# Optimization experiments

Hardware: AMD Instinct MI355X
Metric: run time of the kernel (lower is better)

Reference implementation:

```python
import jax, jax.numpy as jnp
import numpy as np

DIM = 1024
N_HEAD = 16
HEAD_DIM = DIM // N_HEAD
HIDDEN = 4 * DIM
EPS = 1e-6
NEG = -1e9


def setup_inputs() -> dict:
    key = jax.random.key(0)
    ks = jax.random.split(key, 9)
    B, T = 2, 2048
    x = jax.random.normal(ks[0], (B, T, DIM), dtype=jnp.float32)
    # additive causal mask [T, T]
    mask = jnp.where(jnp.tril(jnp.ones((T, T), dtype=bool)), 0.0, NEG).astype(jnp.float32)
    s = 0.02
    wq = jax.random.normal(ks[1], (DIM, DIM), dtype=jnp.float32) * s
    wk = jax.random.normal(ks[2], (DIM, DIM), dtype=jnp.float32) * s
    wv = jax.random.normal(ks[3], (DIM, DIM), dtype=jnp.float32) * s
    wo = jax.random.normal(ks[4], (DIM, DIM), dtype=jnp.float32) * s
    w1 = jax.random.normal(ks[5], (DIM, HIDDEN), dtype=jnp.float32) * s
    w2 = jax.random.normal(ks[6], (HIDDEN, DIM), dtype=jnp.float32) * s
    g_attn = jnp.ones((DIM,), dtype=jnp.float32)
    g_ffn = jnp.ones((DIM,), dtype=jnp.float32)
    return {"x": x, "mask": mask, "wq": wq, "wk": wk, "wv": wv, "wo": wo,
            "w1": w1, "w2": w2, "g_attn": g_attn, "g_ffn": g_ffn}


def _rmsnorm(x, g):
    norm = jax.lax.rsqrt(jnp.mean(jnp.square(x), axis=-1, keepdims=True) + EPS)
    return (x * norm) * g


def _attention(x, mask, wq, wk, wv, wo):
    B, T, C = x.shape
    # project and split heads: [B, H, T, D]
    q = (x @ wq).reshape(B, T, N_HEAD, HEAD_DIM).transpose(0, 2, 1, 3)
    k = (x @ wk).reshape(B, T, N_HEAD, HEAD_DIM).transpose(0, 2, 1, 3)
    v = (x @ wv).reshape(B, T, N_HEAD, HEAD_DIM).transpose(0, 2, 1, 3)
    attn = jnp.einsum('bhtd,bhsd->bhts', q, k) / np.sqrt(HEAD_DIM).astype(np.float32)
    attn = attn + mask  # broadcast [T,T] over [B,H,T,T]
    p = jax.nn.softmax(attn, axis=-1)
    out = jnp.einsum('bhts,bhsd->bhtd', p, v)
    out = out.transpose(0, 2, 1, 3).reshape(B, T, C)
    return out @ wo


def reference(x, mask, wq, wk, wv, wo, w1, w2, g_attn, g_ffn):
    x = x + _attention(_rmsnorm(x, g_attn), mask, wq, wk, wv, wo)
    h = _rmsnorm(x, g_ffn)
    return x + (jax.nn.silu(h @ w1) @ w2)
```

## Files before the change

### kernel.cpp

```cpp
#include <hip/hip_runtime.h>
#include <hip/hip_bf16.h>
#include <cstdint>
#include <cstddef>

#define DIM    1024
#define NHEAD  16
#define HDIM   64
#define HIDDEN 4096
#define TSEQ   2048
#define TOKENS 4096

typedef __attribute__((ext_vector_type(4))) float  f32x4;
typedef __attribute__((ext_vector_type(8))) short  short8;
typedef __attribute__((ext_vector_type(8))) __bf16 bf16x8;

__device__ __forceinline__ short f2bf(float f) {
    union { float f; uint32_t u; } v; v.f = f;
    uint32_t u = v.u;
    uint32_t r = (u + 0x7fffu + ((u >> 16) & 1u)) >> 16;
    return (short)r;
}

__device__ __forceinline__ float bf2f(short s) {
    uint32_t u = ((uint32_t)(uint16_t)s) << 16;
    return __builtin_bit_cast(float, u);
}

__device__ __forceinline__ f32x4 mfma_bf16(short8 a, short8 b, f32x4 c) {
    return __builtin_amdgcn_mfma_f32_16x16x32_bf16(
        __builtin_bit_cast(bf16x8, a), __builtin_bit_cast(bf16x8, b), c, 0, 0, 0);
}

__device__ __forceinline__ void barrier_lds() {
    asm volatile("s_waitcnt lgkmcnt(0)\n\ts_barrier" ::: "memory");
}

__global__ __launch_bounds__(256) void transpose_w(
    const float* __restrict__ W, short* __restrict__ Wt, int K, int N)
{
    __shared__ float tile[64][65];
    const int tid = threadIdx.x;
    const int n0 = blockIdx.x * 64, k0 = blockIdx.y * 64;
    for (int i = tid; i < 4096; i += 256) {
        int r = i >> 6, c = i & 63;
        tile[r][c] = W[(size_t)(k0 + r) * N + n0 + c];
    }
    __syncthreads();
    for (int i = tid; i < 4096; i += 256) {
        int r = i >> 6, c = i & 63;
        Wt[(size_t)(n0 + r) * K + k0 + c] = f2bf(tile[c][r]);
    }
}

__global__ __launch_bounds__(256) void transpose_v(
    const short* __restrict__ qkv, short* __restrict__ Vt)
{
    __shared__ short tile[64][72];
    const int tid = threadIdx.x;
    const int s0 = blockIdx.x * 64, bh = blockIdx.y;
    const int b = bh >> 4, h = bh & 15;
    const short* src = qkv + ((size_t)(b * TSEQ + s0)) * 3072 + 2048 + h * 64;
    for (int i = tid; i < 512; i += 256) {
        int r = i >> 3, cg = i & 7;
        *(short8*)&tile[r][cg * 8] = *(const short8*)(src + (size_t)r * 3072 + cg * 8);
    }
    __syncthreads();
    short* dst = Vt + ((size_t)bh * 64) * TSEQ + s0;
    for (int i = tid; i < 512; i += 256) {
        int d = i >> 3, sg = i & 7;
        short8 o;
#pragma unroll
        for (int j = 0; j < 8; ++j) o[j] = tile[sg * 8 + j][d];
        *(short8*)(dst + (size_t)d * TSEQ + sg * 8) = o;
    }
}

__global__ __launch_bounds__(256) void rmsnorm_k(
    const float* __restrict__ x, const float* __restrict__ g, short* __restrict__ out)
{
    const int t = blockIdx.x, tid = threadIdx.x;
    const int wave = tid >> 6, lane = tid & 63;
    const float4 v = ((const float4*)(x + (size_t)t * DIM))[tid];
    float ss = v.x * v.x + v.y * v.y + v.z * v.z + v.w * v.w;
#pragma unroll
    for (int d = 1; d < 64; d <<= 1) ss += __shfl_xor(ss, d, 64);
    __shared__ float red[4];
    if (lane == 0) red[wave] = ss;
    __syncthreads();
    float tot = red[0] + red[1] + red[2] + red[3];
    float rn = rsqrtf(tot * (1.0f / (float)DIM) + 1e-6f);
    const float4 gv = ((const float4*)g)[tid];
    short4 ov = make_short4(f2bf(v.x * rn * gv.x), f2bf(v.y * rn * gv.y),
                            f2bf(v.z * rn * gv.z), f2bf(v.w * rn * gv.w));
    ((short4*)(out + (size_t)t * DIM))[tid] = ov;
}

template <int EPI>
__global__ __launch_bounds__(256) void gemm_bt(
    const short* __restrict__ A, const short* __restrict__ Bt,
    void* __restrict__ Cout, const float* __restrict__ res,
    int M, int N, int K)
{
    __shared__ short As[128 * 64];
    __shared__ short Bs[128 * 64];
    const int tid  = threadIdx.x;
    const int wave = tid >> 6, lane = tid & 63;
    const int lm = lane & 15, quad = lane >> 4;
    const int wm = wave & 1, wn = wave >> 1;
    const int m0 = blockIdx.x * 128, n0 = blockIdx.y * 128;
    const int Ksl = K / gridDim.z;
    const int kbeg = blockIdx.z * Ksl;
    const int nIter = Ksl >> 6;

    const f32x4 zero = {0.f, 0.f, 0.f, 0.f};
    f32x4 acc[4][4];
#pragma unroll
    for (int i = 0; i < 4; ++i)
#pragma unroll
        for (int j = 0; j < 4; ++j) acc[i][j] = zero;

    const int srow = tid >> 3;
    const int scol = (tid & 7) * 8;
    const int pcol = ((tid & 7) ^ (srow & 7)) * 8;
    const short* Ap = A + (size_t)(m0 + srow) * K + kbeg + scol;
    const short* Bp = Bt + (size_t)(n0 + srow) * K + kbeg + scol;

    short8 ar[4], br[4];

    auto loadtile = [&]() {
#pragma unroll
        for (int j = 0; j < 4; ++j) {
            ar[j] = *(const short8*)(Ap + (size_t)(j * 32) * K);
            br[j] = *(const short8*)(Bp + (size_t)(j * 32) * K);
        }
        Ap += 64; Bp += 64;
    };

    auto storetile = [&]() {
#pragma unroll
        for (int j = 0; j < 4; ++j) {
            *(short8*)&As[(srow + j * 32) * 64 + pcol] = ar[j];
            *(short8*)&Bs[(srow + j * 32) * 64 + pcol] = br[j];
        }
    };

    const int e = lm & 7;
    auto compute = [&]() {
#pragma unroll
        for (int kk = 0; kk < 2; ++kk) {
            short8 af[4], bf[4];
#pragma unroll
            for (int mt = 0; mt < 4; ++mt)
                af[mt] = *(const short8*)&As[(wm * 64 + mt * 16 + lm) * 64 +
                                             ((((kk << 2) | quad) ^ e) << 3)];
#pragma unroll
            for (int nt = 0; nt < 4; ++nt)
                bf[nt] = *(const short8*)&Bs[(wn * 64 + nt * 16 + lm) * 64 +
                                             ((((kk << 2) | quad) ^ e) << 3)];
#pragma unroll
            for (int mt = 0; mt < 4; ++mt)
#pragma unroll
                for (int nt = 0; nt < 4; ++nt)
                    acc[mt][nt] = mfma_bf16(af[mt], bf[nt], acc[mt][nt]);
        }
    };

    loadtile();

    for (int it = 0; it < nIter; ++it) {
        barrier_lds();
        storetile();
        barrier_lds();
        if (it + 1 < nIter) loadtile();
        compute();
    }

#pragma unroll
    for (int mt = 0; mt < 4; ++mt) {
#pragma unroll
        for (int r = 0; r < 4; ++r) {
            const int row = m0 + wm * 64 + mt * 16 + quad * 4 + r;
#pragma unroll
            for (int nt = 0; nt < 4; ++nt) {
                const int col = n0 + wn * 64 + nt * 16 + lm;
                const size_t idx = (size_t)row * N + col;
                const float v = acc[mt][nt][r];
                if constexpr (EPI == 0) {
                    ((short*)Cout)[idx] = f2bf(v);
                } else if constexpr (EPI == 1) {
                    ((float*)Cout)[idx] = res[idx] + v;
                } else if constexpr (EPI == 2) {
                    ((short*)Cout)[idx] = f2bf(v / (1.0f + __expf(-v)));
                } else {
                    ((short*)Cout)[(size_t)blockIdx.z * M * N + idx] = f2bf(v);
                }
            }
        }
    }
}

__global__ __launch_bounds__(256) void combine_k4(
    const short* __restrict__ p, const float* __restrict__ res,
    float* __restrict__ out, int n)
{
    const int i = blockIdx.x * 256 + threadIdx.x;
    if (i * 4 < n) {
        float4 v = ((const float4*)res)[i];
#pragma unroll
        for (int s = 0; s < 4; ++s) {
            short4 ps = ((const short4*)(p + (size_t)s * n))[i];
            v.x += bf2f(ps.x); v.y += bf2f(ps.y);
            v.z += bf2f(ps.z); v.w += bf2f(ps.w);
        }
        ((float4*)out)[i] = v;
    }
}

__global__ __launch_bounds__(256) void combine_rms4(
    const short* __restrict__ p, const float* __restrict__ res,
    const float* __restrict__ g, float* __restrict__ x2out,
    short* __restrict__ nout)
{
    const int t = blockIdx.x, tid = threadIdx.x;
    const int wave = tid >> 6, lane = tid & 63;
    const size_t i4 = (size_t)t * 256 + tid;
    float4 v = ((const float4*)res)[i4];
#pragma unroll
    for (int s = 0; s < 4; ++s) {
        short4 ps = ((const short4*)(p + (size_t)s * TOKENS * DIM))[i4];
        v.x += bf2f(ps.x); v.y += bf2f(ps.y);
        v.z += bf2f(ps.z); v.w += bf2f(ps.w);
    }
    ((float4*)x2out)[i4] = v;
    float ss = v.x * v.x + v.y * v.y + v.z * v.z + v.w * v.w;
#pragma unroll
    for (int d = 1; d < 64; d <<= 1) ss += __shfl_xor(ss, d, 64);
    __shared__ float red[4];
    if (lane == 0) red[wave] = ss;
    __syncthreads();
    float tot = red[0] + red[1] + red[2] + red[3];
    float rn = rsqrtf(tot * (1.0f / (float)DIM) + 1e-6f);
    const float4 gv = ((const float4*)g)[tid];
    short4 ov = make_short4(f2bf(v.x * rn * gv.x), f2bf(v.y * rn * gv.y),
                            f2bf(v.z * rn * gv.z), f2bf(v.w * rn * gv.w));
    ((short4*)nout)[i4] = ov;
}

__global__ __launch_bounds__(256, 2) void attn_k(
    const short* __restrict__ qkv, const short* __restrict__ Vt,
    short* __restrict__ out)
{
    __shared__ short Ks[2][64 * 64];
    __shared__ short Vts[2][64 * 64];
    __shared__ short Ps[4][32 * 64];

    const int tid = threadIdx.x, wave = tid >> 6, lane = tid & 63;
    const int pair = wave >> 1, wv = wave & 1;
    const int lm = lane & 15, quad = lane >> 4;
    const int e = lm & 7;
    const int bh = blockIdx.x;
    const int qt = (gridDim.y - 1) - blockIdx.y;
    const int b = bh >> 4, h = bh & 15;
    const int q0 = qt * 64;

    const int n  = qt + 1;
    const int nA = (n + 1) >> 1;
    const int nP = pair ? (n >> 1) : nA;
    const int sbase = pair ? nA : 0;

    const int tp = tid & 127;
    const int rr = tp >> 3, cg = tp & 7;
    const int pcol = (cg ^ (rr & 7)) * 8;

    const short* qb = qkv + ((size_t)(b * TSEQ + q0)) * 3072 + h * 64;
    short8 aq[2][2];
#pragma unroll
    for (int mt = 0; mt < 2; ++mt)
#pragma unroll
        for (int kk = 0; kk < 2; ++kk)
            aq[mt][kk] = *(const short8*)(qb + (size_t)(wv * 32 + mt * 16 + lm) * 3072 + kk * 32 + quad * 8);

    const short* kb  = qkv + (size_t)b * TSEQ * 3072 + 1024 + h * 64;
    const short* vtb = Vt + (size_t)bh * 64 * TSEQ;

    const f32x4 zero = {0.f, 0.f, 0.f, 0.f};
    f32x4 o_acc[2][4];
#pragma unroll
    for (int mt = 0; mt < 2; ++mt)
#pragma unroll
        for (int t = 0; t < 4; ++t) o_acc[mt][t] = zero;
    float lsum[2][4] = {{0.f, 0.f, 0.f, 0.f}, {0.f, 0.f, 0.f, 0.f}};

    short8 kr[4], vr[4];
    if (nP > 0) {
        const size_t s0i = (size_t)sbase * 64;
#pragma unroll
        for (int j = 0; j < 4; ++j) {
            kr[j] = *(const short8*)(kb + (s0i + rr + j * 16) * 3072 + cg * 8);
            vr[j] = *(const short8*)(vtb + (size_t)(rr + j * 16) * TSEQ + s0i + cg * 8);
        }
    }

    for (int it = 0; it < nA; ++it) {
        const int st = sbase + it;
        const bool act = it < nP;
        __syncthreads();
        if (act) {
#pragma unroll
            for (int j = 0; j < 4; ++j) {
                *(short8*)&Ks[pair][(rr + j * 16) * 64 + pcol] = kr[j];
                *(short8*)&Vts[pair][(rr + j * 16) * 64 + pcol] = vr[j];
            }
        }
        __syncthreads();
        if (act && it + 1 < nP) {
            const size_t sn = (size_t)(st + 1) * 64;
#pragma unroll
            for (int j = 0; j < 4; ++j) {
                kr[j] = *(const short8*)(kb + (sn + rr + j * 16) * 3072 + cg * 8);
                vr[j] = *(const short8*)(vtb + (size_t)(rr + j * 16) * TSEQ + sn + cg * 8);
            }
        }
        if (!act) continue;

        f32x4 sa[2][4];
#pragma unroll
        for (int mt = 0; mt < 2; ++mt)
#pragma unroll
            for (int nt = 0; nt < 4; ++nt) sa[mt][nt] = zero;
#pragma unroll
        for (int kk = 0; kk < 2; ++kk) {
#pragma unroll
            for (int nt = 0; nt < 4; ++nt) {
                short8 bk = *(const short8*)&Ks[pair][(nt * 16 + lm) * 64 +
                                                     ((((kk << 2) | quad) ^ e) << 3)];
                sa[0][nt] = mfma_bf16(aq[0][kk], bk, sa[0][nt]);
                sa[1][nt] = mfma_bf16(aq[1][kk], bk, sa[1][nt]);
            }
        }

        const int s0 = st * 64;
        const bool band = (st == qt);
#pragma unroll
        for (int mt = 0; mt < 2; ++mt) {
            const int qrow = q0 + wv * 32 + mt * 16 + quad * 4;
#pragma unroll
            for (int nt = 0; nt < 4; ++nt) {
                const int col = s0 + nt * 16 + lm;
                const int cch = nt * 2 + (lm >> 3);
#pragma unroll
                for (int r = 0; r < 4; ++r) {
                    float p = exp2f(0.18033688011112042f * sa[mt][nt][r]);
                    if (band && col > qrow + r) p = 0.f;
                    lsum[mt][r] += p;
                    const int prow = mt * 16 + quad * 4 + r;
                    Ps[wave][prow * 64 + ((cch ^ (prow & 7)) << 3) + (lm & 7)] =
                        (short)(__builtin_bit_cast(uint32_t, p) >> 16);
                }
            }
        }

#pragma unroll
        for (int kk = 0; kk < 2; ++kk) {
            short8 ap0 = *(const short8*)&Ps[wave][lm * 64 + ((((kk << 2) | quad) ^ e) << 3)];
            short8 ap1 = *(const short8*)&Ps[wave][(16 + lm) * 64 + ((((kk << 2) | quad) ^ e) << 3)];
#pragma unroll
            for (int t = 0; t < 4; ++t) {
                short8 bv = *(const short8*)&Vts[pair][(t * 16 + lm) * 64 +
                                                       ((((kk << 2) | quad) ^ e) << 3)];
                o_acc[0][t] = mfma_bf16(ap0, bv, o_acc[0][t]);
                o_acc[1][t] = mfma_bf16(ap1, bv, o_acc[1][t]);
            }
        }
    }

#pragma unroll
    for (int mt = 0; mt < 2; ++mt)
#pragma unroll
        for (int r = 0; r < 4; ++r) {
            float s = lsum[mt][r];
#pragma unroll
            for (int d = 1; d < 16; d <<= 1) s += __shfl_xor(s, d, 16);
            lsum[mt][r] = s;
        }

    __syncthreads();
    float* Ob = (float*)&Ks[0][0];
    float* Lb = (float*)&Ps[0][0];
    if (pair == 1) {
#pragma unroll
        for (int mt = 0; mt < 2; ++mt)
#pragma unroll
            for (int t = 0; t < 4; ++t)
#pragma unroll
                for (int r = 0; r < 4; ++r)
                    Ob[(wv * 32 + mt * 16 + quad * 4 + r) * 64 + t * 16 + lm] = o_acc[mt][t][r];
        if (lm == 0) {
#pragma unroll
            for (int mt = 0; mt < 2; ++mt)
#pragma unroll
                for (int r = 0; r < 4; ++r)
                    Lb[wv * 32 + mt * 16 + quad * 4 + r] = lsum[mt][r];
        }
    }
    __syncthreads();
    if (pair == 0) {
#pragma unroll
        for (int mt = 0; mt < 2; ++mt) {
#pragma unroll
            for (int r = 0; r < 4; ++r) {
                const int lrow = wv * 32 + mt * 16 + quad * 4 + r;
                float ltot = lsum[mt][r] + Lb[lrow];
                const float inv = 1.0f / ltot;
                const int token = b * TSEQ + q0 + lrow;
#pragma unroll
                for (int t = 0; t < 4; ++t) {
                    float o = o_acc[mt][t][r] + Ob[lrow * 64 + t * 16 + lm];
                    out[(size_t)token * 1024 + h * 64 + t * 16 + lm] = f2bf(o * inv);
                }
            }
        }
    }
}

extern "C" void kernel_launch(void* const* d_in, const int* in_sizes, int n_in,
                              void* d_out, int out_size, void* d_ws, size_t ws_size,
                              hipStream_t stream)
{
    const float* x      = (const float*)d_in[0];
    const float* wq     = (const float*)d_in[2];
    const float* wk     = (const float*)d_in[3];
    const float* wv     = (const float*)d_in[4];
    const float* wo     = (const float*)d_in[5];
    const float* w1     = (const float*)d_in[6];
    const float* w2     = (const float*)d_in[7];
    const float* g_attn = (const float*)d_in[8];
    const float* g_ffn  = (const float*)d_in[9];
    float* out = (float*)d_out;

    char* ws = (char*)d_ws;
    const size_t MB = 1024 * 1024;
    short* Wqkv_t = (short*)(ws + 0);
    short* Wo_t   = (short*)(ws + 6 * MB);
    short* W1_t   = (short*)(ws + 8 * MB);
    short* xn     = (short*)(ws + 16 * MB);
    short* hbuf   = (short*)(ws + 24 * MB);
    short* qkv    = (short*)(ws + 32 * MB);
    short* pbufO  = (short*)(ws + 32 * MB);
    short* Vt     = (short*)(ws + 64 * MB);
    float* x2     = (float*)(ws + 64 * MB);
    short* W2_t   = (short*)(ws + 80 * MB);
    short* pbuf2  = (short*)(ws + 0);

    dim3 blk(256);

    transpose_w<<<dim3(16, 16), blk, 0, stream>>>(wq, Wqkv_t, 1024, 1024);
    transpose_w<<<dim3(16, 16), blk, 0, stream>>>(wk, Wqkv_t + (size_t)1024 * 1024, 1024, 1024);
    transpose_w<<<dim3(16, 16), blk, 0, stream>>>(wv, Wqkv_t + (size_t)2048 * 1024, 1024, 1024);
    transpose_w<<<dim3(16, 16), blk, 0, stream>>>(wo, Wo_t, 1024, 1024);
    transpose_w<<<dim3(64, 16), blk, 0, stream>>>(w1, W1_t, 1024, 4096);
    transpose_w<<<dim3(16, 64), blk, 0, stream>>>(w2, W2_t, 4096, 1024);

    rmsnorm_k<<<TOKENS, blk, 0, stream>>>(x, g_attn, xn);

    gemm_bt<0><<<dim3(TOKENS / 128, 3072 / 128), blk, 0, stream>>>(
        xn, Wqkv_t, qkv, nullptr, TOKENS, 3072, 1024);

    transpose_v<<<dim3(TSEQ / 64, 32), blk, 0, stream>>>(qkv, Vt);

    attn_k<<<dim3(32, TSEQ / 64), dim3(256), 0, stream>>>(qkv, Vt, xn);

    gemm_bt<3><<<dim3(TOKENS / 128, 1024 / 128, 4), blk, 0, stream>>>(
        xn, Wo_t, pbufO, nullptr, TOKENS, 1024, 1024);

    combine_rms4<<<TOKENS, blk, 0, stream>>>(pbufO, x, g_ffn, x2, hbuf);

    gemm_bt<2><<<dim3(TOKENS / 128, HIDDEN / 128), blk, 0, stream>>>(
        hbuf, W1_t, qkv, nullptr, TOKENS, HIDDEN, 1024);

    gemm_bt<3><<<dim3(TOKENS / 128, 1024 / 128, 4), blk, 0, stream>>>(
        qkv, W2_t, pbuf2, nullptr, TOKENS, 1024, HIDDEN);

    combine_k4<<<dim3(TOKENS * DIM / 4 / 256), blk, 0, stream>>>(
        pbuf2, x2, out, TOKENS * DIM);
}
```

Measured before the change: 353.7 us.

## Compute softmax row sums via MFMA with ones, split masked/unmasked paths, pad P

Replaces the per-element scalar row-sum accumulation and the final shuffle reduction with an extra MFMA that multiplies the bf16 P tile by a ones vector. The sums now come from the same rounded P values used in the PV product. The causal mask branch is moved outside the loop, so only the diagonal tile evaluates the comparison. The P shared buffer switches from an XOR-swizzled layout to a padded row stride of 72 to avoid bank conflicts with simpler address arithmetic. This cuts VALU work in the softmax stage at the cost of a few extra MFMAs per tile.

New measurement: 355.4 us. Within noise of the previous version (+0.5%).

```diff
diff --git a/kernel.cpp b/kernel.cpp
--- a/kernel.cpp
+++ b/kernel.cpp
@@ -246,13 +246,14 @@
     ((short4*)nout)[i4] = ov;
 }
 
+#define PLP 72
 __global__ __launch_bounds__(256, 2) void attn_k(
     const short* __restrict__ qkv, const short* __restrict__ Vt,
     short* __restrict__ out)
 {
     __shared__ short Ks[2][64 * 64];
     __shared__ short Vts[2][64 * 64];
-    __shared__ short Ps[4][32 * 64];
+    __shared__ short Ps[4][32 * PLP];
 
     const int tid = threadIdx.x, wave = tid >> 6, lane = tid & 63;
     const int pair = wave >> 1, wv = wave & 1;
@@ -283,13 +284,18 @@
     const short* kb  = qkv + (size_t)b * TSEQ * 3072 + 1024 + h * 64;
     const short* vtb = Vt + (size_t)bh * 64 * TSEQ;
 
+    const short ONEBF = (short)0x3F80;
+    const short8 ones8 = {ONEBF, ONEBF, ONEBF, ONEBF, ONEBF, ONEBF, ONEBF, ONEBF};
+
     const f32x4 zero = {0.f, 0.f, 0.f, 0.f};
     f32x4 o_acc[2][4];
-#pragma unroll
-    for (int mt = 0; mt < 2; ++mt)
+    f32x4 lacc[2];
+#pragma unroll
+    for (int mt = 0; mt < 2; ++mt) {
 #pragma unroll
         for (int t = 0; t < 4; ++t) o_acc[mt][t] = zero;
-    float lsum[2][4] = {{0.f, 0.f, 0.f, 0.f}, {0.f, 0.f, 0.f, 0.f}};
+        lacc[mt] = zero;
+    }
 
     short8 kr[4], vr[4];
     if (nP > 0) {
@@ -340,30 +346,41 @@
         }
 
         const int s0 = st * 64;
-        const bool band = (st == qt);
-#pragma unroll
-        for (int mt = 0; mt < 2; ++mt) {
-            const int qrow = q0 + wv * 32 + mt * 16 + quad * 4;
-#pragma unroll
-            for (int nt = 0; nt < 4; ++nt) {
-                const int col = s0 + nt * 16 + lm;
-                const int cch = nt * 2 + (lm >> 3);
-#pragma unroll
-                for (int r = 0; r < 4; ++r) {
-                    float p = exp2f(0.18033688011112042f * sa[mt][nt][r]);
-                    if (band && col > qrow + r) p = 0.f;
-                    lsum[mt][r] += p;
-                    const int prow = mt * 16 + quad * 4 + r;
-                    Ps[wave][prow * 64 + ((cch ^ (prow & 7)) << 3) + (lm & 7)] =
-                        (short)(__builtin_bit_cast(uint32_t, p) >> 16);
+        if (st != qt) {
+#pragma unroll
+            for (int mt = 0; mt < 2; ++mt)
+#pragma unroll
+                for (int nt = 0; nt < 4; ++nt)
+#pragma unroll
+                    for (int r = 0; r < 4; ++r) {
+                        float p = exp2f(0.18033688011112042f * sa[mt][nt][r]);
+                        Ps[wave][(mt * 16 + quad * 4 + r) * PLP + nt * 16 + lm] =
+                            (short)(__builtin_bit_cast(uint32_t, p) >> 16);
+                    }
+        } else {
+#pragma unroll
+            for (int mt = 0; mt < 2; ++mt) {
+                const int qrow = q0 + wv * 32 + mt * 16 + quad * 4;
+#pragma unroll
+                for (int nt = 0; nt < 4; ++nt) {
+                    const int col = s0 + nt * 16 + lm;
+#pragma unroll
+                    for (int r = 0; r < 4; ++r) {
+                        float p = exp2f(0.18033688011112042f * sa[mt][nt][r]);
+                        if (col > qrow + r) p = 0.f;
+                        Ps[wave][(mt * 16 + quad * 4 + r) * PLP + nt * 16 + lm] =
+                            (short)(__builtin_bit_cast(uint32_t, p) >> 16);
+                    }
                 }
             }
         }
 
 #pragma unroll
         for (int kk = 0; kk < 2; ++kk) {
-            short8 ap0 = *(const short8*)&Ps[wave][lm * 64 + ((((kk << 2) | quad) ^ e) << 3)];
-            short8 ap1 = *(const short8*)&Ps[wave][(16 + lm) * 64 + ((((kk << 2) | quad) ^ e) << 3)];
+            short8 ap0 = *(const short8*)&Ps[wave][lm * PLP + kk * 32 + quad * 8];
+            short8 ap1 = *(const short8*)&Ps[wave][(16 + lm) * PLP + kk * 32 + quad * 8];
+            lacc[0] = mfma_bf16(ap0, ones8, lacc[0]);
+            lacc[1] = mfma_bf16(ap1, ones8, lacc[1]);
 #pragma unroll
             for (int t = 0; t < 4; ++t) {
                 short8 bv = *(const short8*)&Vts[pair][(t * 16 + lm) * 64 +
@@ -374,16 +391,6 @@
         }
     }
 
-#pragma unroll
-    for (int mt = 0; mt < 2; ++mt)
-#pragma unroll
-        for (int r = 0; r < 4; ++r) {
-            float s = lsum[mt][r];
-#pragma unroll
-            for (int d = 1; d < 16; d <<= 1) s += __shfl_xor(s, d, 16);
-            lsum[mt][r] = s;
-        }
-
     __syncthreads();
     float* Ob = (float*)&Ks[0][0];
     float* Lb = (float*)&Ps[0][0];
@@ -400,7 +407,7 @@
             for (int mt = 0; mt < 2; ++mt)
 #pragma unroll
                 for (int r = 0; r < 4; ++r)
-                    Lb[wv * 32 + mt * 16 + quad * 4 + r] = lsum[mt][r];
+                    Lb[wv * 32 + mt * 16 + quad * 4 + r] = lacc[mt][r];
         }
     }
     __syncthreads();
@@ -410,7 +417,7 @@
 #pragma unroll
             for (int r = 0; r < 4; ++r) {
                 const int lrow = wv * 32 + mt * 16 + quad * 4 + r;
-                float ltot = lsum[mt][r] + Lb[lrow];
+                float ltot = lacc[mt][r] + Lb[lrow];
                 const float inv = 1.0f / ltot;
                 const int token = b * TSEQ + q0 + lrow;
 #pragma unroll
```
